# Kernel optimization log

Measured on AMD Instinct MI355X. Metric: run time of the kernel, lower is better.

Reference implementation:

```python
import jax, jax.numpy as jnp
import numpy as np

A = 9          # angRes
MIND = -4      # mindisp
MAXD = 4       # maxdisp
C0 = A // 2
BDR = C0 * MAXD  # per-view zero padding


def setup_inputs() -> dict:
    key = jax.random.key(0)
    k1, k2, k3 = jax.random.split(key, 3)
    b, c, h, w = 1, 32, 192, 192
    cout = 128
    x = jax.random.normal(k1, (b, c, A * A, h, w), dtype=jnp.float32)
    mask = jax.random.uniform(k2, (b, A * A, h, w), dtype=jnp.float32)
    W = jax.random.normal(k3, (cout, A * A), dtype=jnp.float32) / np.sqrt(A * A)
    return {"x": x, "mask": mask, "W": W}


def reference(x, mask, W):
    # x: [b, c, A*A, h, w], mask: [b, A*A, h, w], W: [cout, A*A] (grouped 1x1 conv, groups=c)
    b, c, aa, h, w = x.shape
    m = W.shape[0] // c  # outputs per group
    Wr = W.reshape(c, m, A, A)
    # per-view layout [b, a1, a2, c, h, w], zero-pad spatially by BDR (equivalent to mosaic padding)
    xv = x.reshape(b, c, A, A, h, w).transpose(0, 2, 3, 1, 4, 5)
    xp = jnp.pad(xv, ((0, 0), (0, 0), (0, 0), (0, 0), (BDR, BDR), (BDR, BDR)))
    maskv = mask.reshape(b, A, A, h, w)
    mask_avg = jnp.mean(mask, axis=1)  # [b, h, w]
    ar = jnp.arange(A)
    outs = []
    for d in range(MIND, MAXD + 1):
        # tap (p,q) of the dilated AxA unfold reads padded view (p,q) shifted by start_p/start_q
        starts = C0 * (d - MIND) - ar * d                      # [A]
        ridx = starts[:, None] + jnp.arange(h)[None, :]        # [A, h]
        cidx = starts[:, None] + jnp.arange(w)[None, :]        # [A, w]
        t = jnp.take_along_axis(xp, ridx[None, :, None, None, :, None], axis=4)
        t = jnp.take_along_axis(t, cidx[None, None, :, None, None, :], axis=5)  # [b,A,A,c,h,w]
        # fuse mask modulation + grouped 1x1 conv over the A*A taps
        o = jnp.einsum('bpqchw,bpqhw,cmpq->bcmhw', t, maskv, Wr)
        outs.append(o.reshape(b, c * m, h, w) / mask_avg[:, None, :, :])
    return jnp.stack(outs, axis=2)  # [b, cout, n_disp, h, w]
```

## Files before the change

kernel.cpp:

```cpp
#include <hip/hip_runtime.h>


#define AA   81
#define HH   192
#define WW   192
#define HW   (HH * WW)
#define NC   32
#define MM   4
#define ND   9


__global__ __launch_bounds__(256)
void buildcost_kernel(const float* __restrict__ x,
                      const float* __restrict__ mask,
                      const float* __restrict__ Wt,
                      float* __restrict__ out) {
    __shared__ float wlds[AA * MM];

    const int lin  = blockIdx.x;
    const int xcd  = lin & 7;
    const int slot = lin >> 3;
    const int cgrp = slot / 144;
    const int sp   = slot - cgrp * 144;
    const int c    = xcd + (cgrp << 3);
    const int by   = sp / 12;
    const int bx   = sp - by * 12;

    const int tx = threadIdx.x & 15;
    const int ty = threadIdx.x >> 4;
    const int j  = bx * 16 + tx;
    const int i  = by * 16 + ty;
    const int pix = i * WW + j;

    for (int idx = threadIdx.x; idx < AA * MM; idx += 256) {
        const int t = idx >> 2;
        const int m = idx & 3;
        wlds[idx] = Wt[(c * MM + m) * AA + t];
    }
    __syncthreads();

    const float* __restrict__ xc = x + (size_t)c * AA * HW;

    float acc[ND][MM];
#pragma unroll
    for (int dd = 0; dd < ND; ++dd)
#pragma unroll
        for (int m = 0; m < MM; ++m) acc[dd][m] = 0.f;

    float msum = 0.f;

    const bool interior = (bx >= 1) & (bx <= 10) & (by >= 1) & (by <= 10);

    if (interior) {
        int p = 0, q = 0;
#pragma unroll 1
        for (int t = 0; t < AA; ++t) {
            const float mval = mask[t * HW + pix];
            msum += mval;
            const float4 w4 = *(const float4*)&wlds[t * 4];
            const int kp = 4 - p;
            const int kq = 4 - q;
            const int step = kp * WW + kq;
            const float* __restrict__ base = xc + (size_t)t * HW + pix;
#pragma unroll
            for (int dd = 0; dd < ND; ++dd) {
                const float v = base[(dd - 4) * step];
                const float s = v * mval;
                acc[dd][0] += s * w4.x;
                acc[dd][1] += s * w4.y;
                acc[dd][2] += s * w4.z;
                acc[dd][3] += s * w4.w;
            }
            if (++q == 9) { q = 0; ++p; }
        }
    } else {
        int p = 0, q = 0;
#pragma unroll 1
        for (int t = 0; t < AA; ++t) {
            const float mval = mask[t * HW + pix];
            msum += mval;
            const float4 w4 = *(const float4*)&wlds[t * 4];
            const int kp = 4 - p;
            const int kq = 4 - q;
            const float* __restrict__ xt = xc + (size_t)t * HW;
#pragma unroll
            for (int dd = 0; dd < ND; ++dd) {
                const int d  = dd - 4;
                const int y  = i + kp * d;
                const int xx = j + kq * d;
                float v = 0.f;
                if ((unsigned)y < (unsigned)HH && (unsigned)xx < (unsigned)WW)
                    v = xt[y * WW + xx];
                const float s = v * mval;
                acc[dd][0] += s * w4.x;
                acc[dd][1] += s * w4.y;
                acc[dd][2] += s * w4.z;
                acc[dd][3] += s * w4.w;
            }
            if (++q == 9) { q = 0; ++p; }
        }
    }

    const float inv = (float)AA / msum;

#pragma unroll
    for (int m = 0; m < MM; ++m)
#pragma unroll
        for (int dd = 0; dd < ND; ++dd)
            out[((size_t)(c * MM + m) * ND + dd) * HW + pix] = acc[dd][m] * inv;
}

extern "C" void kernel_launch(void* const* d_in, const int* in_sizes, int n_in,
                              void* d_out, int out_size, void* d_ws, size_t ws_size,
                              hipStream_t stream) {
    const float* x    = (const float*)d_in[0];
    const float* mask = (const float*)d_in[1];
    const float* Wt   = (const float*)d_in[2];
    float* out        = (float*)d_out;

    dim3 grid(12 * 12 * NC);
    dim3 block(256);
    buildcost_kernel<<<grid, block, 0, stream>>>(x, mask, Wt, out);
}
```

Before: 878.1 us.

## Stage 48x48 halo tiles in double-buffered LDS with register prefetch

Each view's 48x48 neighborhood (16-pixel halo around the 16x16 tile) is loaded cooperatively with float4 global loads into a double-buffered LDS tile, then the nine disparity taps are read from LDS instead of from scattered global addresses. The next view's tile and mask value are prefetched into registers during compute of the current one, overlapping latency. The separate interior/border paths merge into one loop, with zero-fill done at staging time. It adds a barrier per view, 18KB+ of LDS per block that may limit occupancy, and redundant halo loading.

```diff
diff --git a/kernel.cpp b/kernel.cpp
--- a/kernel.cpp
+++ b/kernel.cpp
@@ -9,13 +9,16 @@
 #define MM   4
 #define ND   9
 
+#define RG      48
+#define RITEMS  (RG * RG / 4)
 
 __global__ __launch_bounds__(256)
 void buildcost_kernel(const float* __restrict__ x,
                       const float* __restrict__ mask,
                       const float* __restrict__ Wt,
                       float* __restrict__ out) {
-    __shared__ float wlds[AA * MM];
+    __shared__ float  wlds[AA * MM];
+    __shared__ float4 buf[2][RITEMS];
 
     const int lin  = blockIdx.x;
     const int xcd  = lin & 7;
@@ -26,20 +29,59 @@
     const int by   = sp / 12;
     const int bx   = sp - by * 12;
 
-    const int tx = threadIdx.x & 15;
-    const int ty = threadIdx.x >> 4;
-    const int j  = bx * 16 + tx;
-    const int i  = by * 16 + ty;
+    const int tid = threadIdx.x;
+    const int tx  = tid & 15;
+    const int ty  = tid >> 4;
+    const int j   = bx * 16 + tx;
+    const int i   = by * 16 + ty;
     const int pix = i * WW + j;
 
-    for (int idx = threadIdx.x; idx < AA * MM; idx += 256) {
+    for (int idx = tid; idx < AA * MM; idx += 256) {
         const int t = idx >> 2;
         const int m = idx & 3;
         wlds[idx] = Wt[(c * MM + m) * AA + t];
     }
-    __syncthreads();
+
+    const int y0 = by * 16 - 16;
+    const int x0 = bx * 16 - 16;
+
+    int off0, off1, off2;
+    bool v0, v1, v2;
+    {
+        const int i0 = tid,        r0 = i0 / 12, c0 = (i0 - r0 * 12) * 4;
+        const int i1 = tid + 256,  r1 = i1 / 12, c1 = (i1 - r1 * 12) * 4;
+        const int i2 = tid + 512,  r2 = i2 / 12, c2 = (i2 - r2 * 12) * 4;
+        const int gy0 = y0 + r0, gx0 = x0 + c0;
+        const int gy1 = y0 + r1, gx1 = x0 + c1;
+        const int gy2 = y0 + r2, gx2 = x0 + c2;
+        v0 = ((unsigned)gy0 < (unsigned)HH) & ((unsigned)gx0 < (unsigned)WW);
+        v1 = ((unsigned)gy1 < (unsigned)HH) & ((unsigned)gx1 < (unsigned)WW);
+        v2 = (i2 < RITEMS) & ((unsigned)gy2 < (unsigned)HH) & ((unsigned)gx2 < (unsigned)WW);
+        off0 = v0 ? (gy0 * WW + gx0) : 0;
+        off1 = v1 ? (gy1 * WW + gx1) : 0;
+        off2 = v2 ? (gy2 * WW + gx2) : 0;
+    }
+    const bool interior = (bx >= 1) & (bx <= 10) & (by >= 1) & (by <= 10);
 
     const float* __restrict__ xc = x + (size_t)c * AA * HW;
+
+    float4 s0, s1, s2;
+    const float4 zf4 = {0.f, 0.f, 0.f, 0.f};
+
+#define STAGE_LOAD(XT)                                                  \
+    do {                                                                \
+        if (interior) {                                                 \
+            s0 = *(const float4*)((XT) + off0);                         \
+            s1 = *(const float4*)((XT) + off1);                         \
+            s2 = zf4;                                                   \
+            if (tid < 64) s2 = *(const float4*)((XT) + off2);           \
+        } else {                                                        \
+            s0 = zf4; s1 = zf4; s2 = zf4;                               \
+            if (v0) s0 = *(const float4*)((XT) + off0);                 \
+            if (v1) s1 = *(const float4*)((XT) + off1);                 \
+            if (v2) s2 = *(const float4*)((XT) + off2);                 \
+        }                                                               \
+    } while (0)
 
     float acc[ND][MM];
 #pragma unroll
@@ -47,58 +89,59 @@
 #pragma unroll
         for (int m = 0; m < MM; ++m) acc[dd][m] = 0.f;
 
+    const float* __restrict__ xt = xc;
+    STAGE_LOAD(xt);
+    {
+        float4* wb = &buf[0][0];
+        wb[tid]       = s0;
+        wb[tid + 256] = s1;
+        if (tid < 64) wb[tid + 512] = s2;
+    }
+    float mval_next = mask[pix];
+    __syncthreads();
+
+    const int lbase = (ty + 16) * RG + (tx + 16);
     float msum = 0.f;
+    int p = 0, q = 0;
+    int cur = 0;
 
-    const bool interior = (bx >= 1) & (bx <= 10) & (by >= 1) & (by <= 10);
+#pragma unroll 1
+    for (int t = 0; t < AA; ++t) {
+        const float mval = mval_next;
+        const bool  more = (t + 1 < AA);
 
-    if (interior) {
-        int p = 0, q = 0;
-#pragma unroll 1
-        for (int t = 0; t < AA; ++t) {
-            const float mval = mask[t * HW + pix];
-            msum += mval;
-            const float4 w4 = *(const float4*)&wlds[t * 4];
-            const int kp = 4 - p;
-            const int kq = 4 - q;
-            const int step = kp * WW + kq;
-            const float* __restrict__ base = xc + (size_t)t * HW + pix;
+        if (more) {
+            xt += HW;
+            STAGE_LOAD(xt);
+            mval_next = mask[(size_t)(t + 1) * HW + pix];
+        }
+
+        msum += mval;
+        const float4 w4 = *(const float4*)&wlds[t * 4];
+        const int kp = 4 - p;
+        const int kq = 4 - q;
+        const int lstep = kp * RG + kq;
+        const float* lb = (const float*)&buf[cur][0];
+
 #pragma unroll
-            for (int dd = 0; dd < ND; ++dd) {
-                const float v = base[(dd - 4) * step];
-                const float s = v * mval;
-                acc[dd][0] += s * w4.x;
-                acc[dd][1] += s * w4.y;
-                acc[dd][2] += s * w4.z;
-                acc[dd][3] += s * w4.w;
-            }
-            if (++q == 9) { q = 0; ++p; }
+        for (int dd = 0; dd < ND; ++dd) {
+            const float v = lb[lbase + (dd - 4) * lstep];
+            const float s = v * mval;
+            acc[dd][0] += s * w4.x;
+            acc[dd][1] += s * w4.y;
+            acc[dd][2] += s * w4.z;
+            acc[dd][3] += s * w4.w;
         }
-    } else {
-        int p = 0, q = 0;
-#pragma unroll 1
-        for (int t = 0; t < AA; ++t) {
-            const float mval = mask[t * HW + pix];
-            msum += mval;
-            const float4 w4 = *(const float4*)&wlds[t * 4];
-            const int kp = 4 - p;
-            const int kq = 4 - q;
-            const float* __restrict__ xt = xc + (size_t)t * HW;
-#pragma unroll
-            for (int dd = 0; dd < ND; ++dd) {
-                const int d  = dd - 4;
-                const int y  = i + kp * d;
-                const int xx = j + kq * d;
-                float v = 0.f;
-                if ((unsigned)y < (unsigned)HH && (unsigned)xx < (unsigned)WW)
-                    v = xt[y * WW + xx];
-                const float s = v * mval;
-                acc[dd][0] += s * w4.x;
-                acc[dd][1] += s * w4.y;
-                acc[dd][2] += s * w4.z;
-                acc[dd][3] += s * w4.w;
-            }
-            if (++q == 9) { q = 0; ++p; }
+
+        if (more) {
+            float4* wb = &buf[cur ^ 1][0];
+            wb[tid]       = s0;
+            wb[tid + 256] = s1;
+            if (tid < 64) wb[tid + 512] = s2;
         }
+        __syncthreads();
+        cur ^= 1;
+        if (++q == 9) { q = 0; ++p; }
     }
 
     const float inv = (float)AA / msum;
```

New measurement: 770.3 us. 12.3% less time.
